# Kernel optimization log

Measured on AMD Instinct MI355X. Metric: run time of the kernel, lower is better.

The kernel has to match this reference:

```python
import jax, jax.numpy as jnp
import numpy as np
from jax import lax

D_MODEL = 1024
EXPAND = 2
D_INNER = EXPAND * D_MODEL  # 2048
D_STATE = 16
D_CONV = 4
DT_RANK = -(-D_INNER // 16)  # ceil(d_inner/16) = 128
BATCH, SEQLEN = 2, 1024
LN_EPS = 1e-5


def setup_inputs() -> dict:
    key = jax.random.key(0)
    ks = jax.random.split(key, 8)
    s = lambda n: 1.0 / np.sqrt(n)
    x = jax.random.normal(ks[0], (BATCH, SEQLEN, D_MODEL), jnp.float32)
    ln_gamma = jnp.ones((D_MODEL,), jnp.float32)
    ln_beta = jnp.zeros((D_MODEL,), jnp.float32)
    in_proj_w = jax.random.normal(ks[1], (D_MODEL, 2 * D_INNER), jnp.float32) * s(D_MODEL)
    conv_w = jax.random.normal(ks[2], (D_INNER, D_CONV), jnp.float32) * s(D_CONV)
    conv_b = jnp.zeros((D_INNER,), jnp.float32)
    x_proj_w = jax.random.normal(ks[3], (D_INNER, DT_RANK + 2 * D_STATE), jnp.float32) * s(D_INNER)
    dt_proj_w = jax.random.uniform(ks[4], (DT_RANK, D_INNER), jnp.float32,
                                   -DT_RANK ** -0.5, DT_RANK ** -0.5)
    # dt bias init: inverse-softplus of dt ~ LogUniform(1e-3, 1e-1)
    dt = jnp.exp(jax.random.uniform(ks[5], (D_INNER,), jnp.float32)
                 * (np.log(0.1) - np.log(0.001)) + np.log(0.001))
    dt = jnp.clip(dt, 1e-4)
    dt_proj_b = dt + jnp.log(-jnp.expm1(-dt))
    A_log = jnp.log(jnp.tile(jnp.arange(1, D_STATE + 1, dtype=jnp.float32)[None, :],
                             (D_INNER, 1)))  # (D_INNER, D_STATE)
    D_param = jnp.ones((D_INNER,), jnp.float32)
    out_proj_w = jax.random.normal(ks[6], (D_INNER, D_MODEL), jnp.float32) * s(D_INNER)
    return {"x": x, "ln_gamma": ln_gamma, "ln_beta": ln_beta, "in_proj_w": in_proj_w,
            "conv_w": conv_w, "conv_b": conv_b, "x_proj_w": x_proj_w,
            "dt_proj_w": dt_proj_w, "dt_proj_b": dt_proj_b, "A_log": A_log,
            "D_param": D_param, "out_proj_w": out_proj_w}


def _layernorm(x, gamma, beta):
    mu = jnp.mean(x, -1, keepdims=True)
    var = jnp.mean(jnp.square(x - mu), -1, keepdims=True)
    return (x - mu) * lax.rsqrt(var + LN_EPS) * gamma + beta


def reference(x, ln_gamma, ln_beta, in_proj_w, conv_w, conv_b, x_proj_w,
              dt_proj_w, dt_proj_b, A_log, D_param, out_proj_w):
    B, L, _ = x.shape
    residual = x
    h = _layernorm(x, ln_gamma, ln_beta)
    xz = h @ in_proj_w                               # (B, L, 2*Di)
    xb, z = jnp.split(xz, 2, axis=-1)                # each (B, L, Di)

    # Depthwise causal conv1d (left pad d_conv-1, truncate to L)
    xp = jnp.pad(xb, ((0, 0), (D_CONV - 1, 0), (0, 0)))
    xc = sum(xp[:, k:k + L, :] * conv_w[:, k] for k in range(D_CONV)) + conv_b
    xb = jax.nn.silu(xc)                             # (B, L, Di)

    # Selective SSM
    xpj = xb @ x_proj_w                              # (B, L, dt_rank + 2N)
    dt_r = xpj[..., :DT_RANK]
    B_mat = xpj[..., DT_RANK:DT_RANK + D_STATE]      # (B, L, N)
    C_mat = xpj[..., DT_RANK + D_STATE:]             # (B, L, N)
    delta = jax.nn.softplus(dt_r @ dt_proj_w + dt_proj_b)  # (B, L, Di)
    A = -jnp.exp(A_log)                              # (Di, N)
    dA = jnp.exp(delta[..., None] * A)               # (B, L, Di, N)
    dBx = delta[..., None] * B_mat[:, :, None, :] * xb[..., None]  # (B, L, Di, N)

    def step(hcar, inp):
        dA_t, dBx_t, C_t = inp                       # (B,Di,N),(B,Di,N),(B,N)
        hcar = dA_t * hcar + dBx_t
        y_t = jnp.einsum('bdn,bn->bd', hcar, C_t)
        return hcar, y_t

    h0 = jnp.zeros((B, D_INNER, D_STATE), xb.dtype)
    _, ys = lax.scan(step, h0, (dA.transpose(1, 0, 2, 3),
                                dBx.transpose(1, 0, 2, 3),
                                C_mat.transpose(1, 0, 2)))
    y = ys.transpose(1, 0, 2) + xb * D_param         # (B, L, Di)

    y = y * jax.nn.silu(z)
    return y @ out_proj_w + residual
```

## Files before the change

### kernel.cpp

```cpp
#include <hip/hip_runtime.h>
#include <hip/hip_bf16.h>

#define D_MODEL 1024
#define D_INNER 2048
#define NPROJ   4096
#define D_STATE 16
#define DT_RANK 128
#define XPJ_N   160
#define SEQLEN  1024
#define BATCH   2
#define NTOK    2048
#define CHUNK   16
#define NCHUNK  (SEQLEN / CHUNK)
#define LOG2_NCHUNK 6
#define SPLITK  8
#define OP_SPLITK 4

typedef short short8 __attribute__((ext_vector_type(8)));
typedef float f32x4 __attribute__((ext_vector_type(4)));

__device__ __forceinline__ float sigmoidf_(float x) { return 1.f / (1.f + __expf(-x)); }
__device__ __forceinline__ ushort f2bf_bits(float f) {
    __hip_bfloat16 h = __float2bfloat16(f);
    return *(ushort*)&h;
}
__device__ __forceinline__ float bf2f(ushort u) {
    union { unsigned int i; float f; } v;
    v.i = ((unsigned int)u) << 16;
    return v.f;
}
#define LOG2E 1.44269504088896f

__global__ __launch_bounds__(256) void ln_kernel(const float* __restrict__ x,
                                                 const float* __restrict__ g,
                                                 const float* __restrict__ be,
                                                 ushort* __restrict__ hb)
{
    int row = blockIdx.x;
    const float4* xr = (const float4*)(x + (long)row * D_MODEL);
    float4 v = xr[threadIdx.x];
    float s1 = v.x + v.y + v.z + v.w;
    float s2 = v.x*v.x + v.y*v.y + v.z*v.z + v.w*v.w;
    for (int off = 32; off >= 1; off >>= 1) {
        s1 += __shfl_down(s1, off);
        s2 += __shfl_down(s2, off);
    }
    __shared__ float red[8];
    int wid = threadIdx.x >> 6;
    if ((threadIdx.x & 63) == 0) { red[wid] = s1; red[4 + wid] = s2; }
    __syncthreads();
    float mu  = (red[0] + red[1] + red[2] + red[3]) * (1.f / D_MODEL);
    float ex2 = (red[4] + red[5] + red[6] + red[7]) * (1.f / D_MODEL);
    float inv = rsqrtf(ex2 - mu * mu + 1e-5f);
    float4 g4 = ((const float4*)g)[threadIdx.x];
    float4 b4 = ((const float4*)be)[threadIdx.x];
    ushort4 o;
    o.x = f2bf_bits((v.x - mu) * inv * g4.x + b4.x);
    o.y = f2bf_bits((v.y - mu) * inv * g4.y + b4.y);
    o.z = f2bf_bits((v.z - mu) * inv * g4.z + b4.z);
    o.w = f2bf_bits((v.w - mu) * inv * g4.w + b4.w);
    *(ushort4*)(hb + (long)row * D_MODEL + threadIdx.x * 4) = o;
}

__device__ __forceinline__ void transpose_tile(const float* __restrict__ in,
                                               ushort* __restrict__ out,
                                               int R, int C, int cx, int ry)
{
    __shared__ float tile[64][65];
    int c0 = cx * 64, r0 = ry * 64;
    #pragma unroll
    for (int i = 0; i < 16; ++i) {
        int idx = threadIdx.x + i * 256;
        int r = idx >> 6, c = idx & 63;
        tile[r][c] = (r0 + r < R && c0 + c < C) ? in[(long)(r0 + r) * C + (c0 + c)] : 0.f;
    }
    __syncthreads();
    #pragma unroll
    for (int i = 0; i < 16; ++i) {
        int idx = threadIdx.x + i * 256;
        int cc = idx >> 6, rr = idx & 63;
        if (c0 + cc < C && r0 + rr < R)
            out[(long)(c0 + cc) * R + (r0 + rr)] = f2bf_bits(tile[rr][cc]);
    }
}

__global__ __launch_bounds__(256) void transpose_all_kernel(const float* __restrict__ w2,
                                                            ushort* __restrict__ W2T,
                                                            const float* __restrict__ w7,
                                                            ushort* __restrict__ W7T,
                                                            const float* __restrict__ xp,
                                                            ushort* __restrict__ XPT,
                                                            const float* __restrict__ dt,
                                                            ushort* __restrict__ DTT)
{
    int idx = blockIdx.x;
    if (idx < 1024) {
        transpose_tile(w2, W2T, D_MODEL, NPROJ, idx & 63, idx >> 6);
    } else if (idx < 1536) {
        int rel = idx - 1024;
        transpose_tile(w7, W7T, D_INNER, D_MODEL, rel & 15, rel >> 4);
    } else if (idx < 1632) {
        int rel = idx - 1536;
        transpose_tile(xp, XPT, D_INNER, XPJ_N, rel % 3, rel / 3);
    } else {
        int rel = idx - 1632;
        transpose_tile(dt, DTT, DT_RANK, D_INNER, rel & 31, rel >> 5);
    }
}

template <int EPI, int OBF>
__global__ __launch_bounds__(256) void gemm_mfma_kernel(const ushort* __restrict__ A,
                                                        const ushort* __restrict__ Bt,
                                                        const float* __restrict__ bias,
                                                        float* __restrict__ Cf,
                                                        ushort* __restrict__ Cb,
                                                        int M, int N, int K, int lda, int ldb)
{
    long zoff = (long)blockIdx.z;
    A  += zoff * K;
    Bt += zoff * K;
    if (OBF == 0) Cf += zoff * (long)M * N;
    int lin = blockIdx.y * gridDim.x + blockIdx.x;
    int cpx = (gridDim.x * gridDim.y) >> 3;
    lin = (lin & 7) * cpx + (lin >> 3);
    int bx = lin % gridDim.x, by = lin / gridDim.x;
    __shared__ __align__(16) ushort Al[128 * 32];
    __shared__ __align__(16) ushort Bl[128 * 32];
    int tid = threadIdx.x;
    int lane = tid & 63;
    int w = tid >> 6, wr = w >> 1, wc = w & 1;
    int m0 = by * 128, n0 = bx * 128;
    f32x4 acc[4][4];
    #pragma unroll
    for (int m = 0; m < 4; ++m)
        #pragma unroll
        for (int n = 0; n < 4; ++n) acc[m][n] = (f32x4){0.f, 0.f, 0.f, 0.f};
    int l15 = lane & 15, kq = lane >> 4;

    for (int k0 = 0; k0 < K; k0 += 32) {
        #pragma unroll
        for (int i = 0; i < 2; ++i) {
            int s = i * 256 + tid;
            int row = s >> 2, kg = s & 3;
            int kgl = kg ^ ((row >> 1) & 3);
            __builtin_amdgcn_global_load_lds(
                (const __attribute__((address_space(1))) void*)(A + (long)(m0 + row) * lda + k0 + kgl * 8),
                (__attribute__((address_space(3))) void*)(Al + s * 8), 16, 0, 0);
            __builtin_amdgcn_global_load_lds(
                (const __attribute__((address_space(1))) void*)(Bt + (long)(n0 + row) * ldb + k0 + kgl * 8),
                (__attribute__((address_space(3))) void*)(Bl + s * 8), 16, 0, 0);
        }
        __syncthreads();
        short8 af[4], bf[4];
        #pragma unroll
        for (int m = 0; m < 4; ++m) {
            int row = wr * 64 + m * 16 + l15;
            af[m] = *(const short8*)&Al[row * 32 + (kq ^ ((row >> 1) & 3)) * 8];
        }
        #pragma unroll
        for (int n = 0; n < 4; ++n) {
            int row = wc * 64 + n * 16 + l15;
            bf[n] = *(const short8*)&Bl[row * 32 + (kq ^ ((row >> 1) & 3)) * 8];
        }
        #pragma unroll
        for (int m = 0; m < 4; ++m)
            #pragma unroll
            for (int n = 0; n < 4; ++n)
                acc[m][n] = __builtin_amdgcn_mfma_f32_16x16x32_bf16(af[m], bf[n], acc[m][n], 0, 0, 0);
        __syncthreads();
    }
    #pragma unroll
    for (int m = 0; m < 4; ++m) {
        #pragma unroll
        for (int n = 0; n < 4; ++n) {
            #pragma unroll
            for (int r = 0; r < 4; ++r) {
                int row = m0 + wr * 64 + m * 16 + kq * 4 + r;
                int col = n0 + wc * 64 + n * 16 + l15;
                float v = acc[m][n][r];
                if (EPI == 1) {
                    v += bias[col];
                    v = (v > 20.f) ? v : log1pf(__expf(v));
                }
                if (OBF) Cb[(long)row * N + col] = f2bf_bits(v);
                else     Cf[(long)row * N + col] = v;
            }
        }
    }
}

template <int EPI, int OBF>
__global__ __launch_bounds__(256) void gemm_mfma64_kernel(const ushort* __restrict__ A,
                                                          const ushort* __restrict__ Bt,
                                                          const float* __restrict__ bias,
                                                          float* __restrict__ Cf,
                                                          ushort* __restrict__ Cb,
                                                          int M, int N, int K)
{
    int lin = blockIdx.y * gridDim.x + blockIdx.x;
    int cpx = (gridDim.x * gridDim.y) >> 3;
    lin = (lin & 7) * cpx + (lin >> 3);
    int bx = lin % gridDim.x, by = lin / gridDim.x;
    __shared__ __align__(16) ushort Al[128 * 32];
    __shared__ __align__(16) ushort Bl[64 * 32];
    int tid = threadIdx.x;
    int lane = tid & 63;
    int w = tid >> 6, wr = w >> 1, wc = w & 1;
    int m0 = by * 128, n0 = bx * 64;
    f32x4 acc[4][2];
    #pragma unroll
    for (int m = 0; m < 4; ++m)
        #pragma unroll
        for (int n = 0; n < 2; ++n) acc[m][n] = (f32x4){0.f, 0.f, 0.f, 0.f};
    int l15 = lane & 15, kq = lane >> 4;

    for (int k0 = 0; k0 < K; k0 += 32) {
        #pragma unroll
        for (int i = 0; i < 2; ++i) {
            int s = i * 256 + tid;
            int row = s >> 2, kg = s & 3;
            int kgl = kg ^ ((row >> 1) & 3);
            __builtin_amdgcn_global_load_lds(
                (const __attribute__((address_space(1))) void*)(A + (long)(m0 + row) * K + k0 + kgl * 8),
                (__attribute__((address_space(3))) void*)(Al + s * 8), 16, 0, 0);
        }
        {
            int s = tid;
            int row = s >> 2, kg = s & 3;
            int kgl = kg ^ ((row >> 1) & 3);
            __builtin_amdgcn_global_load_lds(
                (const __attribute__((address_space(1))) void*)(Bt + (long)(n0 + row) * K + k0 + kgl * 8),
                (__attribute__((address_space(3))) void*)(Bl + s * 8), 16, 0, 0);
        }
        __syncthreads();
        short8 af[4], bf[2];
        #pragma unroll
        for (int m = 0; m < 4; ++m) {
            int row = wr * 64 + m * 16 + l15;
            af[m] = *(const short8*)&Al[row * 32 + (kq ^ ((row >> 1) & 3)) * 8];
        }
        #pragma unroll
        for (int n = 0; n < 2; ++n) {
            int row = wc * 32 + n * 16 + l15;
            bf[n] = *(const short8*)&Bl[row * 32 + (kq ^ ((row >> 1) & 3)) * 8];
        }
        #pragma unroll
        for (int m = 0; m < 4; ++m)
            #pragma unroll
            for (int n = 0; n < 2; ++n)
                acc[m][n] = __builtin_amdgcn_mfma_f32_16x16x32_bf16(af[m], bf[n], acc[m][n], 0, 0, 0);
        __syncthreads();
    }
    #pragma unroll
    for (int m = 0; m < 4; ++m) {
        #pragma unroll
        for (int n = 0; n < 2; ++n) {
            #pragma unroll
            for (int r = 0; r < 4; ++r) {
                int row = m0 + wr * 64 + m * 16 + kq * 4 + r;
                int col = n0 + wc * 32 + n * 16 + l15;
                float v = acc[m][n][r];
                if (EPI == 1) {
                    v += bias[col];
                    v = (v > 20.f) ? v : log1pf(__expf(v));
                }
                if (OBF) Cb[(long)row * N + col] = f2bf_bits(v);
                else     Cf[(long)row * N + col] = v;
            }
        }
    }
}

__global__ __launch_bounds__(256) void reduce_out_kernel(const float* __restrict__ Ppart,
                                                         const float* __restrict__ resid,
                                                         float* __restrict__ out)
{
    long i = (long)blockIdx.x * 256 + threadIdx.x;
    const long STRIDE = (long)NTOK * D_MODEL / 4;
    float4 s = ((const float4*)Ppart)[i];
    #pragma unroll
    for (int k = 1; k < OP_SPLITK; ++k) {
        float4 p = ((const float4*)Ppart)[k * STRIDE + i];
        s.x += p.x; s.y += p.y; s.z += p.z; s.w += p.w;
    }
    float4 r = ((const float4*)resid)[i];
    s.x += r.x; s.y += r.y; s.z += r.z; s.w += r.w;
    ((float4*)out)[i] = s;
}

__global__ __launch_bounds__(256) void gemm4_mfma_kernel(const ushort* __restrict__ A,
                                                         const ushort* __restrict__ Bt,
                                                         float* __restrict__ Ppart,
                                                         int M, int K)
{
    __shared__ __align__(16) ushort Al[64 * 32];
    __shared__ __align__(16) ushort Bl[160 * 32];
    int tid = threadIdx.x;
    int lane = tid & 63;
    int w = tid >> 6, wr = w >> 1, wc = w & 1;
    int sk = blockIdx.x;
    int m0 = blockIdx.y * 64;
    int kbase = sk * (K / SPLITK);
    f32x4 acc[2][5];
    #pragma unroll
    for (int m = 0; m < 2; ++m)
        #pragma unroll
        for (int n = 0; n < 5; ++n) acc[m][n] = (f32x4){0.f, 0.f, 0.f, 0.f};
    int l15 = lane & 15, kq = lane >> 4;

    for (int ks = 0; ks < K / SPLITK; ks += 32) {
        int k0 = kbase + ks;
        {
            int s = tid;
            int row = s >> 2, kg = s & 3;
            int kgl = kg ^ ((row >> 1) & 3);
            __builtin_amdgcn_global_load_lds(
                (const __attribute__((address_space(1))) void*)(A + (long)(m0 + row) * K + k0 + kgl * 8),
                (__attribute__((address_space(3))) void*)(Al + s * 8), 16, 0, 0);
        }
        #pragma unroll
        for (int i = 0; i < 3; ++i) {
            int s = i * 256 + tid;
            if (s < 640) {
                int row = s >> 2, kg = s & 3;
                int kgl = kg ^ ((row >> 1) & 3);
                __builtin_amdgcn_global_load_lds(
                    (const __attribute__((address_space(1))) void*)(Bt + (long)row * K + k0 + kgl * 8),
                    (__attribute__((address_space(3))) void*)(Bl + s * 8), 16, 0, 0);
            }
        }
        __syncthreads();
        short8 af[2], bf[5];
        #pragma unroll
        for (int m = 0; m < 2; ++m) {
            int row = wr * 32 + m * 16 + l15;
            af[m] = *(const short8*)&Al[row * 32 + (kq ^ ((row >> 1) & 3)) * 8];
        }
        #pragma unroll
        for (int n = 0; n < 5; ++n) {
            int row = wc * 80 + n * 16 + l15;
            bf[n] = *(const short8*)&Bl[row * 32 + (kq ^ ((row >> 1) & 3)) * 8];
        }
        #pragma unroll
        for (int m = 0; m < 2; ++m)
            #pragma unroll
            for (int n = 0; n < 5; ++n)
                acc[m][n] = __builtin_amdgcn_mfma_f32_16x16x32_bf16(af[m], bf[n], acc[m][n], 0, 0, 0);
        __syncthreads();
    }
    float* P = Ppart + (long)sk * M * XPJ_N;
    #pragma unroll
    for (int m = 0; m < 2; ++m) {
        #pragma unroll
        for (int n = 0; n < 5; ++n) {
            #pragma unroll
            for (int r = 0; r < 4; ++r) {
                int row = m0 + wr * 32 + m * 16 + kq * 4 + r;
                int col = wc * 80 + n * 16 + l15;
                P[(long)row * XPJ_N + col] = acc[m][n][r];
            }
        }
    }
}

__global__ __launch_bounds__(256) void reduce_xpj_kernel(const float* __restrict__ Ppart,
                                                         float* __restrict__ xpj,
                                                         ushort* __restrict__ dtr)
{
    long i = (long)blockIdx.x * 256 + threadIdx.x;
    float s = 0.f;
    #pragma unroll
    for (int k = 0; k < SPLITK; ++k) s += Ppart[k * (long)NTOK * XPJ_N + i];
    xpj[i] = s;
    int col = (int)(i % XPJ_N);
    long row = i / XPJ_N;
    if (col < DT_RANK) dtr[row * DT_RANK + col] = f2bf_bits(s);
}

__global__ __launch_bounds__(256) void conv_silu_kernel(const ushort* __restrict__ xzb,
                                                        const float* __restrict__ cw,
                                                        const float* __restrict__ cb,
                                                        ushort* __restrict__ xbb)
{
    long i = (long)blockIdx.x * 256 + threadIdx.x;
    int d = (int)(i & (D_INNER - 1));
    long tok = i >> 11;
    int l = (int)(tok & (SEQLEN - 1));
    float w0 = cw[d * 4 + 0], w1 = cw[d * 4 + 1], w2 = cw[d * 4 + 2], w3 = cw[d * 4 + 3];
    float acc = cb[d];
    acc += bf2f(xzb[tok * NPROJ + d]) * w3;
    if (l >= 1) acc += bf2f(xzb[(tok - 1) * NPROJ + d]) * w2;
    if (l >= 2) acc += bf2f(xzb[(tok - 2) * NPROJ + d]) * w1;
    if (l >= 3) acc += bf2f(xzb[(tok - 3) * NPROJ + d]) * w0;
    float v = acc * sigmoidf_(acc);
    xbb[i] = f2bf_bits(v);
}


__global__ __launch_bounds__(256) void scan_partial_kernel(const ushort* __restrict__ deltab,
                                                           const ushort* __restrict__ xbb,
                                                           const float* __restrict__ xpj,
                                                           const float* __restrict__ A_log,
                                                           float* __restrict__ Pout,
                                                           float* __restrict__ Hout)
{
    __shared__ float bc[CHUNK][32];
    int blk = blockIdx.x;
    int db = blk & 7;
    int c  = (blk >> 3) & (NCHUNK - 1);
    int b  = blk >> (3 + LOG2_NCHUNK);
    int d  = db * 256 + threadIdx.x;
    long tok0 = (long)b * SEQLEN + c * CHUNK;
    for (int i = threadIdx.x; i < CHUNK * 32; i += 256) {
        int t = i >> 5, cc = i & 31;
        bc[t][cc] = xpj[(tok0 + t) * XPJ_N + DT_RANK + cc];
    }
    float a[16], h[16];
    #pragma unroll
    for (int q = 0; q < 4; ++q) {
        float4 al = *(const float4*)&A_log[d * D_STATE + q * 4];
        a[q*4+0] = -__expf(al.x) * LOG2E;
        a[q*4+1] = -__expf(al.y) * LOG2E;
        a[q*4+2] = -__expf(al.z) * LOG2E;
        a[q*4+3] = -__expf(al.w) * LOG2E;
    }
    #pragma unroll
    for (int n = 0; n < 16; ++n) h[n] = 0.f;
    float cum = 0.f;
    const ushort* dp = deltab + tok0 * D_INNER + d;
    const ushort* xp = xbb + tok0 * D_INNER + d;
    __syncthreads();
    for (int t = 0; t < CHUNK; ++t) {
        float dl = bf2f(dp[(long)t * D_INNER]);
        float x  = bf2f(xp[(long)t * D_INNER]);
        float ux = dl * x;
        cum += dl;
        #pragma unroll
        for (int q = 0; q < 4; ++q) {
            float4 Bv = *(const float4*)&bc[t][q * 4];
            h[q*4+0] = exp2f(dl * a[q*4+0]) * h[q*4+0] + ux * Bv.x;
            h[q*4+1] = exp2f(dl * a[q*4+1]) * h[q*4+1] + ux * Bv.y;
            h[q*4+2] = exp2f(dl * a[q*4+2]) * h[q*4+2] + ux * Bv.z;
            h[q*4+3] = exp2f(dl * a[q*4+3]) * h[q*4+3] + ux * Bv.w;
        }
    }
    long chbase = ((long)(b * NCHUNK + c) * D_INNER + d) * D_STATE;
    #pragma unroll
    for (int q = 0; q < 4; ++q) {
        float4 pv = {exp2f(a[q*4+0] * cum), exp2f(a[q*4+1] * cum),
                     exp2f(a[q*4+2] * cum), exp2f(a[q*4+3] * cum)};
        *(float4*)&Pout[chbase + q * 4] = pv;
        float4 hv = {h[q*4+0], h[q*4+1], h[q*4+2], h[q*4+3]};
        *(float4*)&Hout[chbase + q * 4] = hv;
    }
}

__global__ __launch_bounds__(256) void scan_chunkscan_kernel(const float* __restrict__ P,
                                                             const float* __restrict__ H,
                                                             float* __restrict__ hinit)
{
    long i = (long)blockIdx.x * 256 + threadIdx.x;
    int n = (int)(i & (D_STATE - 1));
    int d = (int)((i >> 4) & (D_INNER - 1));
    int b = (int)(i >> 15);
    float h = 0.f;
    for (int c = 0; c < NCHUNK; ++c) {
        long o = ((((long)b * NCHUNK + c) * D_INNER + d) * D_STATE) + n;
        hinit[o] = h;
        h = P[o] * h + H[o];
    }
}

__global__ __launch_bounds__(256) void scan_final_kernel(const ushort* __restrict__ deltab,
                                                         const ushort* __restrict__ xbb,
                                                         const float* __restrict__ xpj,
                                                         const ushort* __restrict__ xzb,
                                                         const float* __restrict__ A_log,
                                                         const float* __restrict__ Dp,
                                                         const float* __restrict__ hinit,
                                                         ushort* __restrict__ yb)
{
    __shared__ float bc[CHUNK][32];
    int blk = blockIdx.x;
    int db = blk & 7;
    int c  = (blk >> 3) & (NCHUNK - 1);
    int b  = blk >> (3 + LOG2_NCHUNK);
    int d  = db * 256 + threadIdx.x;
    long tok0 = (long)b * SEQLEN + c * CHUNK;
    for (int i = threadIdx.x; i < CHUNK * 32; i += 256) {
        int t = i >> 5, cc = i & 31;
        bc[t][cc] = xpj[(tok0 + t) * XPJ_N + DT_RANK + cc];
    }
    float a[16], h[16];
    #pragma unroll
    for (int q = 0; q < 4; ++q) {
        float4 al = *(const float4*)&A_log[d * D_STATE + q * 4];
        a[q*4+0] = -__expf(al.x) * LOG2E;
        a[q*4+1] = -__expf(al.y) * LOG2E;
        a[q*4+2] = -__expf(al.z) * LOG2E;
        a[q*4+3] = -__expf(al.w) * LOG2E;
    }
    long chbase = ((long)(b * NCHUNK + c) * D_INNER + d) * D_STATE;
    #pragma unroll
    for (int q = 0; q < 4; ++q) {
        float4 hv = *(const float4*)&hinit[chbase + q * 4];
        h[q*4+0] = hv.x; h[q*4+1] = hv.y; h[q*4+2] = hv.z; h[q*4+3] = hv.w;
    }
    float dpar = Dp[d];
    const ushort* dp = deltab + tok0 * D_INNER + d;
    const ushort* xp = xbb + tok0 * D_INNER + d;
    const ushort* zp = xzb + tok0 * NPROJ + D_INNER + d;
    ushort* yp = yb + tok0 * D_INNER + d;
    __syncthreads();
    for (int t = 0; t < CHUNK; ++t) {
        float dl = bf2f(dp[(long)t * D_INNER]);
        float x  = bf2f(xp[(long)t * D_INNER]);
        float z  = bf2f(zp[(long)t * NPROJ]);
        float ux = dl * x;
        float y = 0.f;
        #pragma unroll
        for (int q = 0; q < 4; ++q) {
            float4 Bv = *(const float4*)&bc[t][q * 4];
            float4 Cv = *(const float4*)&bc[t][16 + q * 4];
            h[q*4+0] = exp2f(dl * a[q*4+0]) * h[q*4+0] + ux * Bv.x;
            h[q*4+1] = exp2f(dl * a[q*4+1]) * h[q*4+1] + ux * Bv.y;
            h[q*4+2] = exp2f(dl * a[q*4+2]) * h[q*4+2] + ux * Bv.z;
            h[q*4+3] = exp2f(dl * a[q*4+3]) * h[q*4+3] + ux * Bv.w;
            y += h[q*4+0] * Cv.x + h[q*4+1] * Cv.y + h[q*4+2] * Cv.z + h[q*4+3] * Cv.w;
        }
        y += x * dpar;
        yp[(long)t * D_INNER] = f2bf_bits(y * (z * sigmoidf_(z)));
    }
}

extern "C" void kernel_launch(void* const* d_in, const int* in_sizes, int n_in,
                              void* d_out, int out_size, void* d_ws, size_t ws_size,
                              hipStream_t stream) {
    const float* x         = (const float*)d_in[0];
    const float* ln_gamma  = (const float*)d_in[1];
    const float* ln_beta   = (const float*)d_in[2];
    const float* in_proj_w = (const float*)d_in[3];
    const float* conv_w    = (const float*)d_in[4];
    const float* conv_b    = (const float*)d_in[5];
    const float* x_proj_w  = (const float*)d_in[6];
    const float* dt_proj_w = (const float*)d_in[7];
    const float* dt_proj_b = (const float*)d_in[8];
    const float* A_log     = (const float*)d_in[9];
    const float* D_param   = (const float*)d_in[10];
    const float* out_proj_w= (const float*)d_in[11];
    float* out = (float*)d_out;

    float* p = (float*)d_ws;
    ushort* hb      = (ushort*)p; p += 1048576;
    ushort* W2T     = (ushort*)p; p += 2097152;
    ushort* W7T     = (ushort*)p; p += 1048576;
    ushort* XPT     = (ushort*)p; p += 163840;
    ushort* DTT     = (ushort*)p; p += 131072;
    ushort* xz_bf16 = (ushort*)p; p += 4194304;
    ushort* xb_bf16 = (ushort*)p; p += 2097152;
    float*  xpj     = p;          p += 327680;
    ushort* dtr     = (ushort*)p; p += 131072;
    ushort* delta_bf16 = (ushort*)p; p += 2097152;
    float*  Ppart   = p;          p += 2621440;
    float*  Pbuf    = p;          p += 4194304;
    float*  Hbuf    = p;          p += 4194304;
    float*  hinit   = p;          p += 4194304;
    ushort* y_bf16  = (ushort*)p; p += 2097152;
    float*  PpartO  = p;          p += 8388608;

    transpose_all_kernel<<<1696, 256, 0, stream>>>(
        in_proj_w, W2T, out_proj_w, W7T, x_proj_w, XPT, dt_proj_w, DTT);

    ln_kernel<<<NTOK, 256, 0, stream>>>(x, ln_gamma, ln_beta, hb);

    gemm_mfma_kernel<0, 1><<<dim3(NPROJ / 128, NTOK / 128), 256, 0, stream>>>(
        hb, W2T, nullptr, nullptr, xz_bf16, NTOK, NPROJ, D_MODEL, D_MODEL, D_MODEL);

    conv_silu_kernel<<<(NTOK * D_INNER) / 256, 256, 0, stream>>>(
        xz_bf16, conv_w, conv_b, xb_bf16);

    gemm4_mfma_kernel<<<dim3(SPLITK, NTOK / 64), 256, 0, stream>>>(
        xb_bf16, XPT, Ppart, NTOK, D_INNER);
    reduce_xpj_kernel<<<(NTOK * XPJ_N) / 256, 256, 0, stream>>>(Ppart, xpj, dtr);

    gemm_mfma64_kernel<1, 1><<<dim3(D_INNER / 64, NTOK / 128), 256, 0, stream>>>(
        dtr, DTT, dt_proj_b, nullptr, delta_bf16, NTOK, D_INNER, DT_RANK);

    scan_partial_kernel<<<BATCH * NCHUNK * 8, 256, 0, stream>>>(
        delta_bf16, xb_bf16, xpj, A_log, Pbuf, Hbuf);
    scan_chunkscan_kernel<<<(BATCH * D_INNER * D_STATE) / 256, 256, 0, stream>>>(
        Pbuf, Hbuf, hinit);
    scan_final_kernel<<<BATCH * NCHUNK * 8, 256, 0, stream>>>(
        delta_bf16, xb_bf16, xpj, xz_bf16, A_log, D_param, hinit, y_bf16);

    gemm_mfma_kernel<0, 0><<<dim3(D_MODEL / 128, NTOK / 128, OP_SPLITK), 256, 0, stream>>>(
        y_bf16, W7T, nullptr, PpartO, nullptr, NTOK, D_MODEL, D_INNER / OP_SPLITK,
        D_INNER, D_INNER);
    reduce_out_kernel<<<(NTOK * D_MODEL / 4) / 256, 256, 0, stream>>>(PpartO, x, out);
}
```

Measured before the change: 193.2 us.

## Double-buffer LDS tiles in MFMA GEMM kernels with async prefetch

Both bf16 MFMA GEMM kernels now use two LDS buffers. The next K-tile is issued via global_load_lds before computing on the current one, with an explicit s_waitcnt vmcnt to wait only for the older loads. This aims to hide global-memory latency behind MFMA work instead of stalling at every tile. It doubles LDS use per block, which may reduce occupancy, and relies on hand-counted vmcnt values and raw barriers being correct.

```diff
diff --git a/kernel.cpp b/kernel.cpp
--- a/kernel.cpp
+++ b/kernel.cpp
@@ -124,8 +124,8 @@
     int cpx = (gridDim.x * gridDim.y) >> 3;
     lin = (lin & 7) * cpx + (lin >> 3);
     int bx = lin % gridDim.x, by = lin / gridDim.x;
-    __shared__ __align__(16) ushort Al[128 * 32];
-    __shared__ __align__(16) ushort Bl[128 * 32];
+    __shared__ __align__(16) ushort Al[2][128 * 32];
+    __shared__ __align__(16) ushort Bl[2][128 * 32];
     int tid = threadIdx.x;
     int lane = tid & 63;
     int w = tid >> 6, wr = w >> 1, wc = w & 1;
@@ -137,7 +137,7 @@
         for (int n = 0; n < 4; ++n) acc[m][n] = (f32x4){0.f, 0.f, 0.f, 0.f};
     int l15 = lane & 15, kq = lane >> 4;
 
-    for (int k0 = 0; k0 < K; k0 += 32) {
+    auto stage = [&](int buf, int k0) {
         #pragma unroll
         for (int i = 0; i < 2; ++i) {
             int s = i * 256 + tid;
@@ -145,29 +145,44 @@
             int kgl = kg ^ ((row >> 1) & 3);
             __builtin_amdgcn_global_load_lds(
                 (const __attribute__((address_space(1))) void*)(A + (long)(m0 + row) * lda + k0 + kgl * 8),
-                (__attribute__((address_space(3))) void*)(Al + s * 8), 16, 0, 0);
+                (__attribute__((address_space(3))) void*)(Al[buf] + s * 8), 16, 0, 0);
             __builtin_amdgcn_global_load_lds(
                 (const __attribute__((address_space(1))) void*)(Bt + (long)(n0 + row) * ldb + k0 + kgl * 8),
-                (__attribute__((address_space(3))) void*)(Bl + s * 8), 16, 0, 0);
-        }
-        __syncthreads();
+                (__attribute__((address_space(3))) void*)(Bl[buf] + s * 8), 16, 0, 0);
+        }
+    };
+
+    stage(0, 0);
+    int cur = 0;
+    for (int k0 = 0; k0 < K; k0 += 32) {
+        if (k0 + 32 < K) {
+            stage(cur ^ 1, k0 + 32);
+            asm volatile("s_waitcnt vmcnt(4)" ::: "memory");
+        } else {
+            asm volatile("s_waitcnt vmcnt(0)" ::: "memory");
+        }
+        __builtin_amdgcn_s_barrier();
+        asm volatile("" ::: "memory");
         short8 af[4], bf[4];
         #pragma unroll
         for (int m = 0; m < 4; ++m) {
             int row = wr * 64 + m * 16 + l15;
-            af[m] = *(const short8*)&Al[row * 32 + (kq ^ ((row >> 1) & 3)) * 8];
+            af[m] = *(const short8*)&Al[cur][row * 32 + (kq ^ ((row >> 1) & 3)) * 8];
         }
         #pragma unroll
         for (int n = 0; n < 4; ++n) {
             int row = wc * 64 + n * 16 + l15;
-            bf[n] = *(const short8*)&Bl[row * 32 + (kq ^ ((row >> 1) & 3)) * 8];
+            bf[n] = *(const short8*)&Bl[cur][row * 32 + (kq ^ ((row >> 1) & 3)) * 8];
         }
         #pragma unroll
         for (int m = 0; m < 4; ++m)
             #pragma unroll
             for (int n = 0; n < 4; ++n)
                 acc[m][n] = __builtin_amdgcn_mfma_f32_16x16x32_bf16(af[m], bf[n], acc[m][n], 0, 0, 0);
-        __syncthreads();
+        asm volatile("" ::: "memory");
+        __builtin_amdgcn_s_barrier();
+        asm volatile("" ::: "memory");
+        cur ^= 1;
     }
     #pragma unroll
     for (int m = 0; m < 4; ++m) {
@@ -201,8 +216,8 @@
     int cpx = (gridDim.x * gridDim.y) >> 3;
     lin = (lin & 7) * cpx + (lin >> 3);
     int bx = lin % gridDim.x, by = lin / gridDim.x;
-    __shared__ __align__(16) ushort Al[128 * 32];
-    __shared__ __align__(16) ushort Bl[64 * 32];
+    __shared__ __align__(16) ushort Al[2][128 * 32];
+    __shared__ __align__(16) ushort Bl[2][64 * 32];
     int tid = threadIdx.x;
     int lane = tid & 63;
     int w = tid >> 6, wr = w >> 1, wc = w & 1;
@@ -214,7 +229,7 @@
         for (int n = 0; n < 2; ++n) acc[m][n] = (f32x4){0.f, 0.f, 0.f, 0.f};
     int l15 = lane & 15, kq = lane >> 4;
 
-    for (int k0 = 0; k0 < K; k0 += 32) {
+    auto stage = [&](int buf, int k0) {
         #pragma unroll
         for (int i = 0; i < 2; ++i) {
             int s = i * 256 + tid;
@@ -222,7 +237,7 @@
             int kgl = kg ^ ((row >> 1) & 3);
             __builtin_amdgcn_global_load_lds(
                 (const __attribute__((address_space(1))) void*)(A + (long)(m0 + row) * K + k0 + kgl * 8),
-                (__attribute__((address_space(3))) void*)(Al + s * 8), 16, 0, 0);
+                (__attribute__((address_space(3))) void*)(Al[buf] + s * 8), 16, 0, 0);
         }
         {
             int s = tid;
@@ -230,26 +245,41 @@
             int kgl = kg ^ ((row >> 1) & 3);
             __builtin_amdgcn_global_load_lds(
                 (const __attribute__((address_space(1))) void*)(Bt + (long)(n0 + row) * K + k0 + kgl * 8),
-                (__attribute__((address_space(3))) void*)(Bl + s * 8), 16, 0, 0);
-        }
-        __syncthreads();
+                (__attribute__((address_space(3))) void*)(Bl[buf] + s * 8), 16, 0, 0);
+        }
+    };
+
+    stage(0, 0);
+    int cur = 0;
+    for (int k0 = 0; k0 < K; k0 += 32) {
+        if (k0 + 32 < K) {
+            stage(cur ^ 1, k0 + 32);
+            asm volatile("s_waitcnt vmcnt(3)" ::: "memory");
+        } else {
+            asm volatile("s_waitcnt vmcnt(0)" ::: "memory");
+        }
+        __builtin_amdgcn_s_barrier();
+        asm volatile("" ::: "memory");
         short8 af[4], bf[2];
         #pragma unroll
         for (int m = 0; m < 4; ++m) {
             int row = wr * 64 + m * 16 + l15;
-            af[m] = *(const short8*)&Al[row * 32 + (kq ^ ((row >> 1) & 3)) * 8];
+            af[m] = *(const short8*)&Al[cur][row * 32 + (kq ^ ((row >> 1) & 3)) * 8];
         }
         #pragma unroll
         for (int n = 0; n < 2; ++n) {
             int row = wc * 32 + n * 16 + l15;
-            bf[n] = *(const short8*)&Bl[row * 32 + (kq ^ ((row >> 1) & 3)) * 8];
+            bf[n] = *(const short8*)&Bl[cur][row * 32 + (kq ^ ((row >> 1) & 3)) * 8];
         }
         #pragma unroll
         for (int m = 0; m < 4; ++m)
             #pragma unroll
             for (int n = 0; n < 2; ++n)
                 acc[m][n] = __builtin_amdgcn_mfma_f32_16x16x32_bf16(af[m], bf[n], acc[m][n], 0, 0, 0);
-        __syncthreads();
+        asm volatile("" ::: "memory");
+        __builtin_amdgcn_s_barrier();
+        asm volatile("" ::: "memory");
+        cur ^= 1;
     }
     #pragma unroll
     for (int m = 0; m < 4; ++m) {
@@ -395,7 +425,6 @@
     float v = acc * sigmoidf_(acc);
     xbb[i] = f2bf_bits(v);
 }
-
 
 __global__ __launch_bounds__(256) void scan_partial_kernel(const ushort* __restrict__ deltab,
                                                            const ushort* __restrict__ xbb,
```

After: 188.6 us. -2.4%, faster.
